# Kernel tuning notes

Hardware: AMD Instinct MI355X
Metric: run time of the kernel (lower is better)

## Reference

```python
import jax, jax.numpy as jnp
import numpy as np

NUM_HEADS = 8
EMBED_DIM = 512
HEAD_SIZE = EMBED_DIM // NUM_HEADS
B, S = 4, 2048


def setup_inputs() -> dict:
    key = jax.random.key(0)
    ks = jax.random.split(key, 9)
    scale = 1.0 / np.sqrt(HEAD_SIZE)
    return {
        "values": jax.random.normal(ks[0], (B, S, EMBED_DIM), jnp.float32),
        "keys": jax.random.normal(ks[1], (B, S, EMBED_DIM), jnp.float32),
        "query": jax.random.normal(ks[2], (B, S, EMBED_DIM), jnp.float32),
        "mask": jax.random.randint(ks[3], (B, S), 0, 2, jnp.int32),
        # per-head projection weights, nn.Linear convention: y = x @ W.T, W is [out,in]
        "Wv": jax.random.normal(ks[4], (HEAD_SIZE, HEAD_SIZE), jnp.float32) * scale,
        "Wk": jax.random.normal(ks[5], (HEAD_SIZE, HEAD_SIZE), jnp.float32) * scale,
        "Wq": jax.random.normal(ks[6], (HEAD_SIZE, HEAD_SIZE), jnp.float32) * scale,
        "Wo": jax.random.normal(ks[7], (EMBED_DIM, EMBED_DIM), jnp.float32) * (1.0 / np.sqrt(EMBED_DIM)),
        "bo": jax.random.normal(ks[8], (EMBED_DIM,), jnp.float32) * 0.01,
    }


def reference(values, keys, query, mask, Wv, Wk, Wq, Wo, bo):
    b, s, e = query.shape
    h, d = NUM_HEADS, HEAD_SIZE
    # reshape to heads, then shared per-head linear (no bias): x @ W.T
    v = jnp.einsum("bkhd,ed->bkhe", values.reshape(b, s, h, d), Wv)
    k = jnp.einsum("bkhd,ed->bkhe", keys.reshape(b, s, h, d), Wk)
    q = jnp.einsum("bqhd,ed->bqhe", query.reshape(b, s, h, d), Wq)
    # scores [b,h,q,k]
    energy = jnp.einsum("bqhd,bkhd->bhqk", q, k)
    energy = jnp.where(mask[:, None, None, :] == 0, jnp.float32(-1e20), energy)
    # NOTE: original scales by sqrt(embed_dim), not sqrt(head_size)
    attention = jax.nn.softmax(energy / np.sqrt(e).astype(np.float32), axis=3)
    out = jnp.einsum("bhqk,bkhd->bqhd", attention, v).reshape(b, s, e)
    out = out @ Wo.T + bo
    return out, attention
```

## Files before the change

kernel.cpp:

```cpp
#include <hip/hip_runtime.h>
#include <hip/hip_bf16.h>

#define Bn 4
#define Sn 2048
#define Hn 8
#define Dn 64
#define En 512

typedef __attribute__((ext_vector_type(8))) short short8v;
typedef __attribute__((ext_vector_type(4))) float float4v;
typedef __attribute__((ext_vector_type(2))) unsigned int uint2v;

__device__ __forceinline__ short f2bf(float x){
    __hip_bfloat16 h = __float2bfloat16(x);
    return *reinterpret_cast<short*>(&h);
}
__device__ __forceinline__ float bf2f(short s){
    union { unsigned int u; float f; } c;
    c.u = ((unsigned int)(unsigned short)s) << 16;
    return c.f;
}
__device__ __forceinline__ unsigned int pack2(float lo, float hi){
    return (unsigned int)(unsigned short)f2bf(lo) | ((unsigned int)(unsigned short)f2bf(hi) << 16);
}

__global__ __launch_bounds__(256) void wo_cvt_kernel(const float* __restrict__ Wo,
                                                     short* __restrict__ Wob){
    int i = (blockIdx.x * 256 + threadIdx.x) * 4;
    float4 v = *(const float4*)(Wo + i);
    short4 o;
    o.x = f2bf(v.x); o.y = f2bf(v.y); o.z = f2bf(v.z); o.w = f2bf(v.w);
    *(short4*)(Wob + i) = o;
}

__global__ __launch_bounds__(256) void proj_kernel(
    const float* __restrict__ values, const float* __restrict__ keys, const float* __restrict__ query,
    const float* __restrict__ Wv, const float* __restrict__ Wk, const float* __restrict__ Wq,
    short* __restrict__ Qp, short* __restrict__ Kp, short* __restrict__ Vt)
{
    const int sel = blockIdx.z;
    const float* X = (sel == 0) ? values : ((sel == 1) ? keys : query);
    const float* W = (sel == 0) ? Wv : ((sel == 1) ? Wk : Wq);
    const int bh = blockIdx.y;
    const int b = bh >> 3, h = bh & 7;
    const int s0 = blockIdx.x * 64;
    const int wave = threadIdx.x >> 6;
    const int lane = threadIdx.x & 63;
    const int l16 = lane & 15, quad = lane >> 4;

    short8v bw[4][2];
    #pragma unroll
    for (int t = 0; t < 4; t++){
      #pragma unroll
      for (int st = 0; st < 2; st++){
        const float* wp = W + (t*16 + l16)*64 + st*32 + quad*8;
        float4 w0 = *(const float4*)(wp);
        float4 w1 = *(const float4*)(wp + 4);
        short8v f;
        f[0]=f2bf(w0.x); f[1]=f2bf(w0.y); f[2]=f2bf(w0.z); f[3]=f2bf(w0.w);
        f[4]=f2bf(w1.x); f[5]=f2bf(w1.y); f[6]=f2bf(w1.z); f[7]=f2bf(w1.w);
        bw[t][st] = f;
      }
    }

    const int row = s0 + wave*16 + l16;
    short8v fa[2];
    #pragma unroll
    for (int st = 0; st < 2; st++){
        const float* xp = X + ((size_t)b*Sn + row)*En + h*Dn + st*32 + quad*8;
        float4 x0 = *(const float4*)(xp);
        float4 x1 = *(const float4*)(xp + 4);
        short8v f;
        f[0]=f2bf(x0.x); f[1]=f2bf(x0.y); f[2]=f2bf(x0.z); f[3]=f2bf(x0.w);
        f[4]=f2bf(x1.x); f[5]=f2bf(x1.y); f[6]=f2bf(x1.z); f[7]=f2bf(x1.w);
        fa[st] = f;
    }

    if (sel == 0){
        const int rbase = s0 + wave*16 + quad*4;
        #pragma unroll
        for (int t = 0; t < 4; t++){
            float4v a = {0.f,0.f,0.f,0.f};
            a = __builtin_amdgcn_mfma_f32_16x16x32_bf16(fa[0], bw[t][0], a, 0,0,0);
            a = __builtin_amdgcn_mfma_f32_16x16x32_bf16(fa[1], bw[t][1], a, 0,0,0);
            int e = t*16 + l16;
            short4 pk;
            pk.x = f2bf(a[0]); pk.y = f2bf(a[1]); pk.z = f2bf(a[2]); pk.w = f2bf(a[3]);
            *(short4*)(Vt + ((size_t)bh*Dn + e)*Sn + rbase) = pk;
        }
    } else {
        short* dst = (sel == 1) ? Kp : Qp;
        #pragma unroll
        for (int t = 0; t < 4; t++){
            float4v a = {0.f,0.f,0.f,0.f};
            a = __builtin_amdgcn_mfma_f32_16x16x32_bf16(bw[t][0], fa[0], a, 0,0,0);
            a = __builtin_amdgcn_mfma_f32_16x16x32_bf16(bw[t][1], fa[1], a, 0,0,0);
            short4 pk;
            pk.x = f2bf(a[0]); pk.y = f2bf(a[1]); pk.z = f2bf(a[2]); pk.w = f2bf(a[3]);
            *(short4*)(dst + ((size_t)bh*Sn + row)*Dn + t*16 + quad*4) = pk;
        }
    }
}

__global__ __launch_bounds__(256, 3) void attn_kernel(
    const short* __restrict__ Qp, const short* __restrict__ Kp, const short* __restrict__ Vt,
    const int* __restrict__ mask, float* __restrict__ attn, short* __restrict__ Obf)
{
    __shared__ short sc[4][16][264];
    __shared__ float wsum[4][16];
    __shared__ float vinv[16];

    const int qt = blockIdx.x, h = blockIdx.y, b = blockIdx.z;
    const int bh = b*Hn + h;
    const int tid = threadIdx.x;
    const int wave = tid >> 6, lane = tid & 63;
    const int l16 = lane & 15, quad = lane >> 4;
    const int q0 = qt * 16;

    const short* Qbase = Qp + (size_t)bh*Sn*Dn;
    const short* Kbase = Kp + (size_t)bh*Sn*Dn;
    const short* Vbase = Vt + (size_t)bh*Dn*Sn;

    short8v qa0 = *(const short8v*)(Qbase + (q0 + l16)*Dn + quad*8);
    short8v qa1 = *(const short8v*)(Qbase + (q0 + l16)*Dn + 32 + quad*8);

    const float SCALE = 0.0441941738241592f;
    const int kw = wave * 512;
    const int km = b*Sn;

    unsigned int pk[32][2];
    float rs = 0.f;
    #pragma unroll
    for (int t = 0; t < 32; t++){
        const int k0 = kw + t*16;
        short8v kb0 = *(const short8v*)(Kbase + (k0 + l16)*Dn + quad*8);
        short8v kb1 = *(const short8v*)(Kbase + (k0 + l16)*Dn + 32 + quad*8);
        float4v a = {0.f,0.f,0.f,0.f};
        a = __builtin_amdgcn_mfma_f32_16x16x32_bf16(kb0, qa0, a, 0,0,0);
        a = __builtin_amdgcn_mfma_f32_16x16x32_bf16(kb1, qa1, a, 0,0,0);
        const int4 mk = *(const int4*)(mask + km + k0 + quad*4);
        float p0 = mk.x ? __expf(a[0]*SCALE) : 0.f;
        float p1 = mk.y ? __expf(a[1]*SCALE) : 0.f;
        float p2 = mk.z ? __expf(a[2]*SCALE) : 0.f;
        float p3 = mk.w ? __expf(a[3]*SCALE) : 0.f;
        rs += (p0 + p1) + (p2 + p3);
        pk[t][0] = pack2(p0, p1);
        pk[t][1] = pack2(p2, p3);
    }

    rs += __shfl_xor(rs, 16);
    rs += __shfl_xor(rs, 32);
    if (lane < 16) wsum[wave][lane] = rs;
    __syncthreads();
    const float stot = wsum[0][l16] + wsum[1][l16] + wsum[2][l16] + wsum[3][l16];
    const float vq = (stot > 0.f) ? 1.f/stot : 0.f;
    if (tid < 16) vinv[tid] = vq;

    float* arow = attn + (size_t)bh*Sn*Sn + (size_t)(q0 + l16)*Sn + kw + quad*4;
    #pragma unroll
    for (int t = 0; t < 32; t++){
        float4v o;
        o[0] = bf2f((short)(pk[t][0] & 0xffff)) * vq;
        o[1] = bf2f((short)(pk[t][0] >> 16))    * vq;
        o[2] = bf2f((short)(pk[t][1] & 0xffff)) * vq;
        o[3] = bf2f((short)(pk[t][1] >> 16))    * vq;
        __builtin_nontemporal_store(o, (float4v*)(arow + t*16));
    }

    float4v acc0 = {0.f,0.f,0.f,0.f}, acc1 = {0.f,0.f,0.f,0.f},
            acc2 = {0.f,0.f,0.f,0.f}, acc3 = {0.f,0.f,0.f,0.f};
    short* scw = &sc[wave][0][0];
    #pragma unroll
    for (int c = 0; c < 2; c++){
        #pragma unroll
        for (int tc = 0; tc < 16; tc++){
            uint2v w2;
            w2[0] = pk[c*16 + tc][0];
            w2[1] = pk[c*16 + tc][1];
            *(uint2v*)(scw + l16*264 + tc*16 + quad*4) = w2;
        }
        #pragma unroll
        for (int ks = 0; ks < 8; ks++){
            const int kv = kw + c*256 + ks*32 + quad*8;
            short8v pa  = *(const short8v*)(scw + l16*264 + ks*32 + quad*8);
            short8v vb0 = *(const short8v*)(Vbase + (size_t)( 0 + l16)*Sn + kv);
            short8v vb1 = *(const short8v*)(Vbase + (size_t)(16 + l16)*Sn + kv);
            short8v vb2 = *(const short8v*)(Vbase + (size_t)(32 + l16)*Sn + kv);
            short8v vb3 = *(const short8v*)(Vbase + (size_t)(48 + l16)*Sn + kv);
            acc0 = __builtin_amdgcn_mfma_f32_16x16x32_bf16(vb0, pa, acc0, 0,0,0);
            acc1 = __builtin_amdgcn_mfma_f32_16x16x32_bf16(vb1, pa, acc1, 0,0,0);
            acc2 = __builtin_amdgcn_mfma_f32_16x16x32_bf16(vb2, pa, acc2, 0,0,0);
            acc3 = __builtin_amdgcn_mfma_f32_16x16x32_bf16(vb3, pa, acc3, 0,0,0);
        }
    }

    __syncthreads();
    float* osc = (float*)&sc[0][0][0];
    {
        float* orow = osc + (wave*16 + l16)*68 + quad*4;
        *(float4v*)(orow +  0) = acc0;
        *(float4v*)(orow + 16) = acc1;
        *(float4v*)(orow + 32) = acc2;
        *(float4v*)(orow + 48) = acc3;
    }
    __syncthreads();
    {
        const int row = tid >> 4, dbase = (tid & 15)*4;
        float4v v =  *(const float4v*)(osc + ( 0 + row)*68 + dbase);
        v = v + *(const float4v*)(osc + (16 + row)*68 + dbase);
        v = v + *(const float4v*)(osc + (32 + row)*68 + dbase);
        v = v + *(const float4v*)(osc + (48 + row)*68 + dbase);
        const float s = vinv[row];
        short4 o;
        o.x = f2bf(v[0]*s); o.y = f2bf(v[1]*s); o.z = f2bf(v[2]*s); o.w = f2bf(v[3]*s);
        *(short4*)(Obf + ((size_t)b*Sn + q0 + row)*En + h*Dn + dbase) = o;
    }
}

__global__ __launch_bounds__(256) void outproj_kernel(
    const short* __restrict__ Obf, const short* __restrict__ Wob,
    const float* __restrict__ bo, float* __restrict__ out)
{
    const int nt = blockIdx.x;
    const int mt = blockIdx.y;
    const int wave = threadIdx.x >> 6, lane = threadIdx.x & 63;
    const int l16 = lane & 15, quad = lane >> 4;
    const int m0 = mt*64 + wave*16;
    const int n0 = nt*64;

    float4v acc0 = {0.f,0.f,0.f,0.f}, acc1 = {0.f,0.f,0.f,0.f},
            acc2 = {0.f,0.f,0.f,0.f}, acc3 = {0.f,0.f,0.f,0.f};
    for (int ks = 0; ks < 16; ks++){
        const int kb = ks*32 + quad*8;
        short8v af = *(const short8v*)(Obf + (size_t)(m0 + l16)*En + kb);
        short8v b0 = *(const short8v*)(Wob + (size_t)(n0 +  0 + l16)*En + kb);
        short8v b1 = *(const short8v*)(Wob + (size_t)(n0 + 16 + l16)*En + kb);
        short8v b2 = *(const short8v*)(Wob + (size_t)(n0 + 32 + l16)*En + kb);
        short8v b3 = *(const short8v*)(Wob + (size_t)(n0 + 48 + l16)*En + kb);
        acc0 = __builtin_amdgcn_mfma_f32_16x16x32_bf16(af, b0, acc0, 0,0,0);
        acc1 = __builtin_amdgcn_mfma_f32_16x16x32_bf16(af, b1, acc1, 0,0,0);
        acc2 = __builtin_amdgcn_mfma_f32_16x16x32_bf16(af, b2, acc2, 0,0,0);
        acc3 = __builtin_amdgcn_mfma_f32_16x16x32_bf16(af, b3, acc3, 0,0,0);
    }
    #pragma unroll
    for (int t = 0; t < 4; t++){
        float4v a = (t==0)?acc0:((t==1)?acc1:((t==2)?acc2:acc3));
        const int e = n0 + t*16 + l16;
        const float bias = bo[e];
        #pragma unroll
        for (int r = 0; r < 4; r++)
            out[(size_t)(m0 + quad*4 + r)*En + e] = a[r] + bias;
    }
}

extern "C" void kernel_launch(void* const* d_in, const int* in_sizes, int n_in,
                              void* d_out, int out_size, void* d_ws, size_t ws_size,
                              hipStream_t stream)
{
    const float* values = (const float*)d_in[0];
    const float* keys   = (const float*)d_in[1];
    const float* query  = (const float*)d_in[2];
    const int*   mask   = (const int*)d_in[3];
    const float* Wv = (const float*)d_in[4];
    const float* Wk = (const float*)d_in[5];
    const float* Wq = (const float*)d_in[6];
    const float* Wo = (const float*)d_in[7];
    const float* bo = (const float*)d_in[8];

    float* out  = (float*)d_out;
    float* attn = out + (size_t)Bn*Sn*En;

    short* Qp  = (short*)d_ws;
    short* Kp  = Qp + (size_t)Bn*Hn*Sn*Dn;
    short* Vt  = Kp + (size_t)Bn*Hn*Sn*Dn;
    short* Obf = Vt + (size_t)Bn*Hn*Sn*Dn;
    short* Wob = Obf + (size_t)Bn*Sn*En;

    wo_cvt_kernel<<<dim3((En*En)/1024), 256, 0, stream>>>(Wo, Wob);
    proj_kernel<<<dim3(Sn/64, Bn*Hn, 3), 256, 0, stream>>>(values, keys, query, Wv, Wk, Wq, Qp, Kp, Vt);
    attn_kernel<<<dim3(Sn/16, Hn, Bn), 256, 0, stream>>>(Qp, Kp, Vt, mask, attn, Obf);
    outproj_kernel<<<dim3(En/64, (Bn*Sn)/64), 256, 0, stream>>>(Obf, Wob, bo, out);
}
```

Before: 882.2 us.

## Recompute normalized scores in a second pass instead of caching probabilities in registers

The attention kernel no longer keeps 64 packed bf16 probabilities per lane in registers. After the row sums are reduced, it recomputes QK^T and exp a second time. It multiplies each value by the inverse sum, stores it to the attention output, and feeds it straight into the PV MFMAs in 128-key chunks through a smaller LDS tile. This lowers register and LDS use so launch bounds can rise from 3 to 5 blocks per CU, and it drops the final rescale and one barrier. In exchange, the K reads, QK MFMAs and exponentials are done twice.

```diff
diff --git a/kernel.cpp b/kernel.cpp
--- a/kernel.cpp
+++ b/kernel.cpp
@@ -102,13 +102,12 @@
     }
 }
 
-__global__ __launch_bounds__(256, 3) void attn_kernel(
+__global__ __launch_bounds__(256, 5) void attn_kernel(
     const short* __restrict__ Qp, const short* __restrict__ Kp, const short* __restrict__ Vt,
     const int* __restrict__ mask, float* __restrict__ attn, short* __restrict__ Obf)
 {
-    __shared__ short sc[4][16][264];
+    __shared__ short sc[4][16][136];
     __shared__ float wsum[4][16];
-    __shared__ float vinv[16];
 
     const int qt = blockIdx.x, h = blockIdx.y, b = blockIdx.z;
     const int bh = b*Hn + h;
@@ -128,7 +127,6 @@
     const int kw = wave * 512;
     const int km = b*Sn;
 
-    unsigned int pk[32][2];
     float rs = 0.f;
     #pragma unroll
     for (int t = 0; t < 32; t++){
@@ -144,8 +142,6 @@
         float p2 = mk.z ? __expf(a[2]*SCALE) : 0.f;
         float p3 = mk.w ? __expf(a[3]*SCALE) : 0.f;
         rs += (p0 + p1) + (p2 + p3);
-        pk[t][0] = pack2(p0, p1);
-        pk[t][1] = pack2(p2, p3);
     }
 
     rs += __shfl_xor(rs, 16);
@@ -154,35 +150,38 @@
     __syncthreads();
     const float stot = wsum[0][l16] + wsum[1][l16] + wsum[2][l16] + wsum[3][l16];
     const float vq = (stot > 0.f) ? 1.f/stot : 0.f;
-    if (tid < 16) vinv[tid] = vq;
-
-    float* arow = attn + (size_t)bh*Sn*Sn + (size_t)(q0 + l16)*Sn + kw + quad*4;
-    #pragma unroll
-    for (int t = 0; t < 32; t++){
-        float4v o;
-        o[0] = bf2f((short)(pk[t][0] & 0xffff)) * vq;
-        o[1] = bf2f((short)(pk[t][0] >> 16))    * vq;
-        o[2] = bf2f((short)(pk[t][1] & 0xffff)) * vq;
-        o[3] = bf2f((short)(pk[t][1] >> 16))    * vq;
-        __builtin_nontemporal_store(o, (float4v*)(arow + t*16));
-    }
 
     float4v acc0 = {0.f,0.f,0.f,0.f}, acc1 = {0.f,0.f,0.f,0.f},
             acc2 = {0.f,0.f,0.f,0.f}, acc3 = {0.f,0.f,0.f,0.f};
     short* scw = &sc[wave][0][0];
-    #pragma unroll
-    for (int c = 0; c < 2; c++){
-        #pragma unroll
-        for (int tc = 0; tc < 16; tc++){
+    float* arow = attn + (size_t)bh*Sn*Sn + (size_t)(q0 + l16)*Sn + kw + quad*4;
+    #pragma unroll
+    for (int c = 0; c < 4; c++){
+        #pragma unroll
+        for (int tc = 0; tc < 8; tc++){
+            const int t = c*8 + tc;
+            const int k0 = kw + t*16;
+            short8v kb0 = *(const short8v*)(Kbase + (k0 + l16)*Dn + quad*8);
+            short8v kb1 = *(const short8v*)(Kbase + (k0 + l16)*Dn + 32 + quad*8);
+            float4v a = {0.f,0.f,0.f,0.f};
+            a = __builtin_amdgcn_mfma_f32_16x16x32_bf16(kb0, qa0, a, 0,0,0);
+            a = __builtin_amdgcn_mfma_f32_16x16x32_bf16(kb1, qa1, a, 0,0,0);
+            const int4 mk = *(const int4*)(mask + km + k0 + quad*4);
+            float p0 = mk.x ? __expf(a[0]*SCALE)*vq : 0.f;
+            float p1 = mk.y ? __expf(a[1]*SCALE)*vq : 0.f;
+            float p2 = mk.z ? __expf(a[2]*SCALE)*vq : 0.f;
+            float p3 = mk.w ? __expf(a[3]*SCALE)*vq : 0.f;
+            float4v o = {p0, p1, p2, p3};
+            __builtin_nontemporal_store(o, (float4v*)(arow + t*16));
             uint2v w2;
-            w2[0] = pk[c*16 + tc][0];
-            w2[1] = pk[c*16 + tc][1];
-            *(uint2v*)(scw + l16*264 + tc*16 + quad*4) = w2;
-        }
-        #pragma unroll
-        for (int ks = 0; ks < 8; ks++){
-            const int kv = kw + c*256 + ks*32 + quad*8;
-            short8v pa  = *(const short8v*)(scw + l16*264 + ks*32 + quad*8);
+            w2[0] = pack2(p0, p1);
+            w2[1] = pack2(p2, p3);
+            *(uint2v*)(scw + l16*136 + tc*16 + quad*4) = w2;
+        }
+        #pragma unroll
+        for (int ks = 0; ks < 4; ks++){
+            const int kv = kw + c*128 + ks*32 + quad*8;
+            short8v pa  = *(const short8v*)(scw + l16*136 + ks*32 + quad*8);
             short8v vb0 = *(const short8v*)(Vbase + (size_t)( 0 + l16)*Sn + kv);
             short8v vb1 = *(const short8v*)(Vbase + (size_t)(16 + l16)*Sn + kv);
             short8v vb2 = *(const short8v*)(Vbase + (size_t)(32 + l16)*Sn + kv);
@@ -194,7 +193,6 @@
         }
     }
 
-    __syncthreads();
     float* osc = (float*)&sc[0][0][0];
     {
         float* orow = osc + (wave*16 + l16)*68 + quad*4;
@@ -210,9 +208,8 @@
         v = v + *(const float4v*)(osc + (16 + row)*68 + dbase);
         v = v + *(const float4v*)(osc + (32 + row)*68 + dbase);
         v = v + *(const float4v*)(osc + (48 + row)*68 + dbase);
-        const float s = vinv[row];
         short4 o;
-        o.x = f2bf(v[0]*s); o.y = f2bf(v[1]*s); o.z = f2bf(v[2]*s); o.w = f2bf(v[3]*s);
+        o.x = f2bf(v[0]); o.y = f2bf(v[1]); o.z = f2bf(v[2]); o.w = f2bf(v[3]);
         *(short4*)(Obf + ((size_t)b*Sn + q0 + row)*En + h*Dn + dbase) = o;
     }
 }
```

After: 964.3 us. 9.3% more time.
